# Kernel optimization log

Measured on AMD Instinct MI355X. Metric: run time of the kernel, lower is better.

## Reference

```python
import jax, jax.numpy as jnp
import numpy as np
import math

# Product of P Lorentz hyperboloids, each of dim D (time coord first), curvature c (K = 1/c).
N, P, D = 30000, 4, 64   # nodes, sub-manifolds, dim per sub-manifold
E = 480000               # edges (COO sparse adjacency)
C_IN, C_OUT = 1.0, 1.0
MIN_NORM = 1e-15
EPS = 1e-7
MAX_NORM = 1000.0


def _arcosh(x):
    return jnp.log(x + jnp.sqrt(jnp.maximum(x * x - 1.0, MIN_NORM)))


def proj(x, K):
    # project onto hyperboloid: recompute time coordinate from space coords
    y = x[..., 1:]
    t = jnp.sqrt(jnp.maximum(K + jnp.sum(y * y, -1, keepdims=True), EPS))
    return jnp.concatenate([t, y], -1)


def proj_tan0(u):
    # tangent space at origin: zero out the time coordinate
    return jnp.concatenate([jnp.zeros_like(u[..., :1]), u[..., 1:]], -1)


def proj_tan(u, x, K):
    ux = jnp.sum(x[..., 1:] * u[..., 1:], -1, keepdims=True)
    t = ux / jnp.maximum(x[..., :1], MIN_NORM)
    return jnp.concatenate([t, u[..., 1:]], -1)


def expmap0(u, K):
    sqrtK = K ** 0.5
    sp = u[..., 1:]
    n = jnp.maximum(jnp.linalg.norm(sp, axis=-1, keepdims=True), MIN_NORM)
    theta = n / sqrtK
    time = sqrtK * jnp.cosh(theta)
    space = sqrtK * jnp.sinh(theta) * sp / n
    return proj(jnp.concatenate([time, space], -1), K)


def logmap0(x, K):
    sqrtK = K ** 0.5
    sp = x[..., 1:]
    n = jnp.maximum(jnp.linalg.norm(sp, axis=-1, keepdims=True), MIN_NORM)
    theta = jnp.maximum(x[..., :1] / sqrtK, 1.0 + EPS)
    space = sqrtK * _arcosh(theta) * sp / n
    return jnp.concatenate([jnp.zeros_like(theta), space], -1)


def mink_dot(x, y):
    return jnp.sum(x[..., 1:] * y[..., 1:], -1, keepdims=True) - x[..., :1] * y[..., :1]


def expmap(u, x, K):
    sqrtK = K ** 0.5
    normu = jnp.minimum(jnp.sqrt(jnp.maximum(mink_dot(u, u), EPS)), MAX_NORM)
    theta = jnp.maximum(normu / sqrtK, MIN_NORM)
    return proj(jnp.cosh(theta) * x + jnp.sinh(theta) * u / theta, K)


def ptransp0(x, u, K):
    # parallel transport of tangent u at origin to point x
    sqrtK = K ** 0.5
    x0 = x[..., :1]
    y = x[..., 1:]
    yn = jnp.maximum(jnp.linalg.norm(y, axis=-1, keepdims=True), MIN_NORM)
    yu = y / yn
    v = jnp.concatenate([-yn, (sqrtK - x0) * yu], -1)
    alpha = jnp.sum(yu * u[..., 1:], -1, keepdims=True) / sqrtK
    return proj_tan(u - alpha * v, x, K)


def mobius_add(x, y, K):
    return expmap(ptransp0(x, logmap0(y, K), K), x, K)


def setup_inputs() -> dict:
    key = jax.random.key(0)
    k1, k2, k3, k4, k5 = jax.random.split(key, 5)
    K = 1.0 / C_IN
    # valid points on the product manifold: expmap0 of random tangent vectors
    t = 0.1 * jax.random.normal(k1, (N, P, D), dtype=jnp.float32)
    x = proj(expmap0(proj_tan0(t), K), K).reshape(N, P * D)
    adj_row = jax.random.randint(k2, (E,), 0, N)
    adj_col = jax.random.randint(k3, (E,), 0, N)
    # roughly degree-normalized positive adjacency weights
    adj_val = jax.random.uniform(k4, (E,), dtype=jnp.float32) / 16.0
    fan = P * D
    gain = math.sqrt(2.0) * math.sqrt(2.0 / (fan + fan))  # xavier_uniform(gain=sqrt(2)) scale
    weight = gain * jax.random.normal(k5, (fan, fan), dtype=jnp.float32)
    bias = jnp.full((fan,), 1e-4, dtype=jnp.float32)  # init.constant_(bias, 0.0001)
    return {"x": x, "adj_val": adj_val, "weight": weight, "bias": bias,
            "adj_row": adj_row, "adj_col": adj_col}


def reference(x, adj_val, weight, bias, adj_row, adj_col):
    K = 1.0 / C_IN
    Ko = 1.0 / C_OUT
    xs = x.reshape(N, P, D)

    # ---- ProLinear: mobius_matvec + hyperbolic bias add ----
    u = logmap0(xs, K).reshape(N, P * D)          # tangent at origin, concat across sub-manifolds
    mu = (u @ weight.T).reshape(N, P, D)          # [N, P*D] @ [P*D, P*D]^T
    h = proj(expmap0(proj_tan0(mu), K), K)
    b = bias.reshape(1, P, D)
    hyp_bias = proj(expmap0(proj_tan0(b), K), K)
    h = proj(mobius_add(h, hyp_bias, K), K)

    # ---- ProAgg: logmap0 -> spmm -> clamp -> expmap0 ----
    xt = logmap0(h, K).reshape(N, P * D)
    msgs = adj_val[:, None] * xt[adj_col]          # [E, P*D] gather
    support = jax.ops.segment_sum(msgs, adj_row, num_segments=N)
    support = jnp.minimum(support, MAX_NORM).reshape(N, P, D)
    h = proj(expmap0(proj_tan0(support), K), K)

    # ---- ProAct: logmap0 (c_in) -> clamped relu -> expmap0 (c_out) ----
    t = logmap0(h, K)
    t = jnp.minimum(jax.nn.relu(t), MAX_NORM)
    out = expmap0(proj_tan0(t), Ko)
    return out.reshape(N, P * D)
```

## Files before the change

kernel.cpp:

```cpp
#include <hip/hip_runtime.h>
#include <hip/hip_bf16.h>

#define MIN_NORM 1e-15f
#define EPS 1e-7f
#define MAX_NORM 1000.0f

#define NN 30000
#define PP 4
#define DD 64
#define EE 480000

typedef __attribute__((ext_vector_type(8))) short short8v;
typedef __attribute__((ext_vector_type(4))) float float4v;

__device__ inline float frcp(float x) { return __builtin_amdgcn_rcpf(x); }
__device__ inline float bf2f(unsigned short u) { return __uint_as_float(((unsigned)u) << 16); }
__device__ inline unsigned short f2bf(float f) {
    unsigned u = __float_as_uint(f);
    return (unsigned short)((u + 0x7fffu + ((u >> 16) & 1u)) >> 16);
}

__device__ inline float wsum(float v) {
#pragma unroll
    for (int off = 32; off >= 1; off >>= 1) v += __shfl_xor(v, off, 64);
    return v;
}
__device__ inline float expmap0_proj_pt(float v, int lane) {
    float sp = (lane == 0) ? 0.f : v;
    float n2 = wsum(sp * sp);
    float n = fmaxf(sqrtf(n2), MIN_NORM);
    float ep = __expf(n), em = frcp(ep);
    float s = 0.5f * (ep - em) * frcp(n);
    float time = sqrtf(fmaxf(1.f + s * s * n2, EPS));
    return (lane == 0) ? time : s * sp;
}
__device__ inline float logmap0_pt(float x, int lane) {
    float sp = (lane == 0) ? 0.f : x;
    float n2 = wsum(sp * sp);
    float n = fmaxf(sqrtf(n2), MIN_NORM);
    float x0 = __shfl(x, 0, 64);
    float th = fmaxf(x0, 1.f + EPS);
    float ac = __logf(th + sqrtf(fmaxf(th * th - 1.f, MIN_NORM)));
    return (lane == 0) ? 0.f : (ac * sp * frcp(n));
}
__device__ inline float gsum16(float v) {
#pragma unroll
    for (int off = 8; off >= 1; off >>= 1) v += __shfl_xor(v, off, 64);
    return v;
}
__device__ inline void gsum16x4(float& a, float& b, float& c, float& d) {
#pragma unroll
    for (int off = 8; off >= 1; off >>= 1) {
        a += __shfl_xor(a, off, 64);
        b += __shfl_xor(b, off, 64);
        c += __shfl_xor(c, off, 64);
        d += __shfl_xor(d, off, 64);
    }
}

__global__ void prep_kernel(const float* __restrict__ w,
                            unsigned short* __restrict__ bhi,
                            unsigned short* __restrict__ blo,
                            int* __restrict__ cz) {
    int b = blockIdx.x;
    if (b < 32) {
        int tt = b * 256 + threadIdx.x;
        int lane = tt & 63;
        int ks = (tt >> 6) & 7;
        int nt = tt >> 9;
        int col = nt * 16 + (lane & 15);
        int kb = ks * 32 + (lane >> 4) * 8;
#pragma unroll
        for (int e = 0; e < 8; e++) {
            float v = w[col * 256 + kb + e];
            unsigned short h = f2bf(v);
            bhi[tt * 8 + e] = h;
            blo[tt * 8 + e] = f2bf(v - bf2f(h));
        }
    } else {
        int i = (b - 32) * 256 + threadIdx.x;
        if (i < 2 * NN) cz[i] = 0;
    }
}

#define GR 16
#define UPITCH 264
__global__ __launch_bounds__(256) void fused_front_hist_kernel(const float* __restrict__ x,
                                                               const unsigned short* __restrict__ bhi,
                                                               const unsigned short* __restrict__ blo,
                                                               const float* __restrict__ bias,
                                                               unsigned short* __restrict__ xt,
                                                               const int* __restrict__ adj_row,
                                                               int* __restrict__ counts,
                                                               int nFront) {
    __shared__ __align__(16) char smem[17952];

    if (blockIdx.x >= nFront) {
        int e = (blockIdx.x - nFront) * 256 + threadIdx.x;
        if (e < EE) atomicAdd(&counts[adj_row[e]], 1);
        return;
    }

    unsigned short* uh = (unsigned short*)smem;
    unsigned short* ul = (unsigned short*)(smem + 8448);
    float* uspL = (float*)(smem + 16896);
    float* u2L  = (float*)(smem + 17920);

    int tid = threadIdx.x;
    int lane = tid & 63;
    int wv = tid >> 6;
    int row0 = blockIdx.x * GR;

    {
        float b = bias[wv * 64 + lane];
        float y = expmap0_proj_pt(b, lane);
        float usp = logmap0_pt(y, lane);
        float U2 = wsum(usp * usp);
        uspL[wv * 64 + lane] = usp;
        if (lane == 0) u2L[wv] = U2;
    }

    int r = tid >> 4, l = tid & 15;
    {
        const float4* xr = (const float4*)(x + (size_t)(row0 + r) * 256);
        float4 a[4];
#pragma unroll
        for (int p = 0; p < 4; p++) a[p] = xr[p * 16 + l];
        float s0, s1, s2, s3;
        {
            float m0 = (l == 0) ? 0.f : a[0].x;
            float m1 = (l == 0) ? 0.f : a[1].x;
            float m2 = (l == 0) ? 0.f : a[2].x;
            float m3 = (l == 0) ? 0.f : a[3].x;
            s0 = m0 * m0 + a[0].y * a[0].y + a[0].z * a[0].z + a[0].w * a[0].w;
            s1 = m1 * m1 + a[1].y * a[1].y + a[1].z * a[1].z + a[1].w * a[1].w;
            s2 = m2 * m2 + a[2].y * a[2].y + a[2].z * a[2].z + a[2].w * a[2].w;
            s3 = m3 * m3 + a[3].y * a[3].y + a[3].z * a[3].z + a[3].w * a[3].w;
        }
        gsum16x4(s0, s1, s2, s3);
        float n2a[4] = {s0, s1, s2, s3};
#pragma unroll
        for (int p = 0; p < 4; p++) {
            float n2 = n2a[p];
            float n = fmaxf(sqrtf(n2), MIN_NORM);
            float th = fmaxf(sqrtf(1.f + n2), 1.f + EPS);
            float ac = __logf(th + sqrtf(fmaxf(th * th - 1.f, MIN_NORM)));
            float sc = ac * frcp(n);
            float ux0 = (l == 0) ? 0.f : sc * a[p].x;
            float uy = sc * a[p].y, uz = sc * a[p].z, uw = sc * a[p].w;
            unsigned short hx = f2bf(ux0), hy = f2bf(uy), hz = f2bf(uz), hw = f2bf(uw);
            ushort4 hv = {hx, hy, hz, hw};
            ushort4 lv = {f2bf(ux0 - bf2f(hx)), f2bf(uy - bf2f(hy)),
                          f2bf(uz - bf2f(hz)), f2bf(uw - bf2f(hw))};
            *(ushort4*)(uh + r * UPITCH + p * 64 + 4 * l) = hv;
            *(ushort4*)(ul + r * UPITCH + p * 64 + 4 * l) = lv;
        }
    }
    __syncthreads();

    float4v acc[4];
#pragma unroll
    for (int j = 0; j < 4; j++) acc[j] = (float4v){0.f, 0.f, 0.f, 0.f};
    int abyte = (lane & 15) * (UPITCH * 2) + (lane >> 4) * 16;
#pragma unroll
    for (int ks = 0; ks < 8; ks++) {
        short8v Ah = *(const short8v*)(smem + abyte + ks * 64);
        short8v Al = *(const short8v*)(smem + 8448 + abyte + ks * 64);
#pragma unroll
        for (int j = 0; j < 4; j++) {
            size_t chunk = ((size_t)((wv * 4 + j) * 8 + ks) * 64 + lane) * 8;
            short8v Bh = *(const short8v*)(bhi + chunk);
            short8v Bl = *(const short8v*)(blo + chunk);
            acc[j] = __builtin_amdgcn_mfma_f32_16x16x32_bf16(Ah, Bh, acc[j], 0, 0, 0);
            acc[j] = __builtin_amdgcn_mfma_f32_16x16x32_bf16(Al, Bh, acc[j], 0, 0, 0);
            acc[j] = __builtin_amdgcn_mfma_f32_16x16x32_bf16(Ah, Bl, acc[j], 0, 0, 0);
        }
    }

    int lp = lane & 15, hi = lane >> 4;
    float uf[4];
#pragma unroll
    for (int j = 0; j < 4; j++) uf[j] = uspL[wv * 64 + j * 16 + lp];
    if (lp == 0) {
        acc[0][0] = 0.f; acc[0][1] = 0.f; acc[0][2] = 0.f; acc[0][3] = 0.f;
    }
    float n2v[4], duv[4];
#pragma unroll
    for (int reg = 0; reg < 4; reg++) {
        float pn = 0.f, pd = 0.f;
#pragma unroll
        for (int j = 0; j < 4; j++) {
            pn = fmaf(acc[j][reg], acc[j][reg], pn);
            pd = fmaf(acc[j][reg], uf[j], pd);
        }
        n2v[reg] = pn; duv[reg] = pd;
    }
#pragma unroll
    for (int off = 1; off < 16; off <<= 1) {
#pragma unroll
        for (int reg = 0; reg < 4; reg++) {
            n2v[reg] += __shfl_xor(n2v[reg], off, 64);
            duv[reg] += __shfl_xor(duv[reg], off, 64);
        }
    }
    float U2 = u2L[wv];

    float A[4], Bc[4];
#pragma unroll
    for (int reg = 0; reg < 4; reg++) {
        float n2 = n2v[reg], duu = duv[reg];
        float n = fmaxf(sqrtf(n2), MIN_NORM);
        float epv = __expf(n), emv = frcp(epv);
        float sv = 0.5f * (epv - emv) * frcp(n);
        float hs2 = sv * sv * n2;
        float h0 = sqrtf(fmaxf(1.f + hs2, EPS));
        float yn = fmaxf(sv * n, MIN_NORM);
        float dhu = sv * duu;
        float alpha = dhu * frcp(yn);
        float g = alpha * (1.f - h0);
        float ux = dhu - g * yn;
        float t = ux * frcp(fmaxf(h0, MIN_NORM));
        float w2 = U2 - 2.f * g * alpha + g * g;
        float md = w2 - t * t;
        float normu = fminf(sqrtf(fmaxf(md, EPS)), MAX_NORM);
        float theta = fmaxf(normu, MIN_NORM);
        float ep2 = __expf(theta), em2 = frcp(ep2);
        float ch = 0.5f * (ep2 + em2);
        float shot = 0.5f * (ep2 - em2) * frcp(theta);
        float rn2 = ch * ch * hs2 + 2.f * ch * shot * ux + shot * shot * w2;
        float rtime = sqrtf(fmaxf(1.f + rn2, EPS));
        float th2 = fmaxf(rtime, 1.f + EPS);
        float ac2 = __logf(th2 + sqrtf(fmaxf(th2 * th2 - 1.f, MIN_NORM)));
        float rn = fmaxf(sqrtf(rn2), MIN_NORM);
        float K = ac2 * frcp(rn);
        A[reg] = K * sv * (ch - shot * g * frcp(yn));
        Bc[reg] = K * shot;
    }

    unsigned short* xbase = xt + (size_t)(row0 + hi * 4) * 256 + wv * 64 + lp;
#pragma unroll
    for (int reg = 0; reg < 4; reg++) {
#pragma unroll
        for (int j = 0; j < 4; j++) {
            float o = fmaf(A[reg], acc[j][reg], Bc[reg] * uf[j]);
            xbase[reg * 256 + j * 16] = f2bf(o);
        }
    }
}

#define SCH 32
__global__ __launch_bounds__(1024) void scan_kernel(const int* __restrict__ counts,
                                                    int* __restrict__ starts, int n) {
    int tid = threadIdx.x, lane = tid & 63, wv = tid >> 6;
    int i0 = tid * SCH;
    int c[SCH];
    const int4* c4 = (const int4*)(counts + i0);
#pragma unroll
    for (int q = 0; q < 8; q++) {
        int4 v = c4[q];
        c[4 * q] = v.x; c[4 * q + 1] = v.y; c[4 * q + 2] = v.z; c[4 * q + 3] = v.w;
    }
    int s = 0;
#pragma unroll
    for (int j = 0; j < SCH; j++) s += c[j];
    int incl = s;
#pragma unroll
    for (int off = 1; off < 64; off <<= 1) {
        int t = __shfl_up(incl, off, 64);
        if (lane >= off) incl += t;
    }
    __shared__ int wtot[16];
    if (lane == 63) wtot[wv] = incl;
    __syncthreads();
    if (wv == 0 && lane < 16) {
        int v = wtot[lane];
        int sc = v;
#pragma unroll
        for (int off = 1; off < 16; off <<= 1) {
            int t = __shfl_up(sc, off, 64);
            if (lane >= off) sc += t;
        }
        wtot[lane] = sc - v;
    }
    __syncthreads();
    int run = incl - s + wtot[wv];
#pragma unroll
    for (int j = 0; j < SCH; j++) {
        int idx = i0 + j;
        if (idx < n) starts[idx] = run;
        run += c[j];
    }
    if (tid == 1023) starts[n] = run;
}

__global__ void scatter_kernel(const int* __restrict__ row, const int* __restrict__ col,
                               const float* __restrict__ val, const int* __restrict__ starts,
                               int* __restrict__ cursor, int2* __restrict__ ep, int E) {
    int e = blockIdx.x * 256 + threadIdx.x;
    if (e < E) {
        int r = row[e];
        int pos = starts[r] + atomicAdd(&cursor[r], 1);
        ep[pos] = make_int2(col[e], __float_as_int(val[e]));
    }
}

__global__ __launch_bounds__(256) void spmm_final_kernel(const unsigned short* __restrict__ xt,
                                                         const int2* __restrict__ ep,
                                                         const int* __restrict__ starts,
                                                         float4* __restrict__ out4) {
    int w = threadIdx.x >> 6;
    int lane = threadIdx.x & 63;
    int r = blockIdx.x * 4 + w;
    int s = starts[r], e = starts[r + 1];

    float4 acc = {0.f, 0.f, 0.f, 0.f};
    for (int i = s; i < e; i += 8) {
        int cs[8]; float vs[8];
#pragma unroll
        for (int u = 0; u < 8; u++) {
            int idx = i + u;
            bool ok = idx < e;
            int2 pe = ep[ok ? idx : s];
            cs[u] = pe.x;
            vs[u] = ok ? __int_as_float(pe.y) : 0.f;
        }
        ushort4 av[8];
#pragma unroll
        for (int u = 0; u < 8; u++)
            av[u] = *(const ushort4*)(xt + ((size_t)cs[u] << 8) + (lane << 2));
#pragma unroll
        for (int u = 0; u < 8; u++) {
            acc.x = fmaf(vs[u], bf2f(av[u].x), acc.x);
            acc.y = fmaf(vs[u], bf2f(av[u].y), acc.y);
            acc.z = fmaf(vs[u], bf2f(av[u].z), acc.z);
            acc.w = fmaf(vs[u], bf2f(av[u].w), acc.w);
        }
    }

    acc.x = fminf(acc.x, MAX_NORM); acc.y = fminf(acc.y, MAX_NORM);
    acc.z = fminf(acc.z, MAX_NORM); acc.w = fminf(acc.w, MAX_NORM);

    bool leader = ((lane & 15) == 0);
    float4 sp = acc;
    if (leader) sp.x = 0.f;
    float n2 = gsum16(sp.x * sp.x + sp.y * sp.y + sp.z * sp.z + sp.w * sp.w);
    float n = fmaxf(sqrtf(n2), MIN_NORM);
    float ep1 = __expf(n), em1 = frcp(ep1);
    float s1 = 0.5f * (ep1 - em1) * frcp(n);
    float hs2 = s1 * s1 * n2;
    float time = sqrtf(fmaxf(1.f + hs2, EPS));
    float th = fmaxf(time, 1.f + EPS);
    float ac = __logf(th + sqrtf(fmaxf(th * th - 1.f, MIN_NORM)));
    float hn = fmaxf(s1 * n, MIN_NORM);
    float sc = ac * s1 * frcp(hn);
    float4 t;
    t.x = leader ? 0.f : sc * sp.x;
    t.y = sc * sp.y;
    t.z = sc * sp.z;
    t.w = sc * sp.w;
    t.x = fminf(fmaxf(t.x, 0.f), MAX_NORM);
    t.y = fminf(fmaxf(t.y, 0.f), MAX_NORM);
    t.z = fminf(fmaxf(t.z, 0.f), MAX_NORM);
    t.w = fminf(fmaxf(t.w, 0.f), MAX_NORM);
    float t2 = gsum16(t.x * t.x + t.y * t.y + t.z * t.z + t.w * t.w);
    float nt = fmaxf(sqrtf(t2), MIN_NORM);
    float ep3 = __expf(nt), em3 = frcp(ep3);
    float s3 = 0.5f * (ep3 - em3) * frcp(nt);
    float time3 = sqrtf(fmaxf(1.f + s3 * s3 * t2, EPS));
    float4 o;
    o.x = leader ? time3 : s3 * t.x;
    o.y = s3 * t.y;
    o.z = s3 * t.z;
    o.w = s3 * t.w;

    out4[(size_t)r * 64 + lane] = o;
}

extern "C" void kernel_launch(void* const* d_in, const int* in_sizes, int n_in,
                              void* d_out, int out_size, void* d_ws, size_t ws_size,
                              hipStream_t stream) {
    const float* x       = (const float*)d_in[0];
    const float* adj_val = (const float*)d_in[1];
    const float* weight  = (const float*)d_in[2];
    const float* bias    = (const float*)d_in[3];
    const int*   adj_row = (const int*)d_in[4];
    const int*   adj_col = (const int*)d_in[5];

    const int N = NN, E = EE;

    unsigned short* B   = (unsigned short*)d_ws;
    unsigned short* Whi = B + (size_t)N * 256;
    unsigned short* Wlo = Whi + 65536;
    int* counts  = (int*)(Wlo + 65536);
    int* cursor  = counts + N;
    int* starts  = cursor + N;
    int2* ep     = (int2*)(starts + N + 2);

    const int nFront = N / GR;
    const int nHist  = (E + 255) / 256;

    prep_kernel<<<32 + (2 * N + 255) / 256, 256, 0, stream>>>(weight, Whi, Wlo, counts);
    fused_front_hist_kernel<<<nFront + nHist, 256, 0, stream>>>(x, Whi, Wlo, bias, B,
                                                                adj_row, counts, nFront);
    scan_kernel<<<1, 1024, 0, stream>>>(counts, starts, N);
    scatter_kernel<<<(E + 255) / 256, 256, 0, stream>>>(adj_row, adj_col, adj_val,
                                                        starts, cursor, ep, E);
    spmm_final_kernel<<<N / 4, 256, 0, stream>>>(B, ep, starts, (float4*)d_out);
}
```

Before: 146.5 us.

## Process 48 rows per front block and fold histogram into the same blocks

Each front block now handles 48 rows (three 16-row MFMA tiles) instead of 16, so every loaded B fragment of the split-bf16 weight is reused across three A tiles. The separate histogram blocks are removed; each front block instead atomically counts 768 edges (625 blocks x 768 = E exactly). The aim is to cut redundant weight fragment loads and launch fewer blocks, at the cost of about 51 KB of LDS per block, more accumulator registers, and reduced occupancy, with only 625 blocks in flight.

```diff
diff --git a/kernel.cpp b/kernel.cpp
--- a/kernel.cpp
+++ b/kernel.cpp
@@ -83,33 +83,33 @@
     }
 }
 
-#define GR 16
+#define GR 48
 #define UPITCH 264
+#define EPB 768
 __global__ __launch_bounds__(256) void fused_front_hist_kernel(const float* __restrict__ x,
                                                                const unsigned short* __restrict__ bhi,
                                                                const unsigned short* __restrict__ blo,
                                                                const float* __restrict__ bias,
                                                                unsigned short* __restrict__ xt,
                                                                const int* __restrict__ adj_row,
-                                                               int* __restrict__ counts,
-                                                               int nFront) {
-    __shared__ __align__(16) char smem[17952];
-
-    if (blockIdx.x >= nFront) {
-        int e = (blockIdx.x - nFront) * 256 + threadIdx.x;
-        if (e < EE) atomicAdd(&counts[adj_row[e]], 1);
-        return;
-    }
-
+                                                               int* __restrict__ counts) {
+    __shared__ __align__(16) char smem[51744];
     unsigned short* uh = (unsigned short*)smem;
-    unsigned short* ul = (unsigned short*)(smem + 8448);
-    float* uspL = (float*)(smem + 16896);
-    float* u2L  = (float*)(smem + 17920);
+    unsigned short* ul = (unsigned short*)(smem + 25344);
+    float* uspL = (float*)(smem + 50688);
+    float* u2L  = (float*)(smem + 51712);
 
     int tid = threadIdx.x;
     int lane = tid & 63;
     int wv = tid >> 6;
-    int row0 = blockIdx.x * GR;
+    int fb = blockIdx.x;
+    int row0 = fb * GR;
+
+    {
+        int e0 = fb * EPB + tid;
+#pragma unroll
+        for (int q = 0; q < 3; q++) atomicAdd(&counts[adj_row[e0 + q * 256]], 1);
+    }
 
     {
         float b = bias[wv * 64 + lane];
@@ -122,58 +122,74 @@
 
     int r = tid >> 4, l = tid & 15;
     {
-        const float4* xr = (const float4*)(x + (size_t)(row0 + r) * 256);
-        float4 a[4];
-#pragma unroll
-        for (int p = 0; p < 4; p++) a[p] = xr[p * 16 + l];
-        float s0, s1, s2, s3;
-        {
-            float m0 = (l == 0) ? 0.f : a[0].x;
-            float m1 = (l == 0) ? 0.f : a[1].x;
-            float m2 = (l == 0) ? 0.f : a[2].x;
-            float m3 = (l == 0) ? 0.f : a[3].x;
-            s0 = m0 * m0 + a[0].y * a[0].y + a[0].z * a[0].z + a[0].w * a[0].w;
-            s1 = m1 * m1 + a[1].y * a[1].y + a[1].z * a[1].z + a[1].w * a[1].w;
-            s2 = m2 * m2 + a[2].y * a[2].y + a[2].z * a[2].z + a[2].w * a[2].w;
-            s3 = m3 * m3 + a[3].y * a[3].y + a[3].z * a[3].z + a[3].w * a[3].w;
-        }
-        gsum16x4(s0, s1, s2, s3);
-        float n2a[4] = {s0, s1, s2, s3};
-#pragma unroll
-        for (int p = 0; p < 4; p++) {
-            float n2 = n2a[p];
-            float n = fmaxf(sqrtf(n2), MIN_NORM);
-            float th = fmaxf(sqrtf(1.f + n2), 1.f + EPS);
-            float ac = __logf(th + sqrtf(fmaxf(th * th - 1.f, MIN_NORM)));
-            float sc = ac * frcp(n);
-            float ux0 = (l == 0) ? 0.f : sc * a[p].x;
-            float uy = sc * a[p].y, uz = sc * a[p].z, uw = sc * a[p].w;
-            unsigned short hx = f2bf(ux0), hy = f2bf(uy), hz = f2bf(uz), hw = f2bf(uw);
-            ushort4 hv = {hx, hy, hz, hw};
-            ushort4 lv = {f2bf(ux0 - bf2f(hx)), f2bf(uy - bf2f(hy)),
-                          f2bf(uz - bf2f(hz)), f2bf(uw - bf2f(hw))};
-            *(ushort4*)(uh + r * UPITCH + p * 64 + 4 * l) = hv;
-            *(ushort4*)(ul + r * UPITCH + p * 64 + 4 * l) = lv;
+        float4 a[3][4];
+#pragma unroll
+        for (int rr = 0; rr < 3; rr++) {
+            const float4* xr = (const float4*)(x + (size_t)(row0 + rr * 16 + r) * 256);
+#pragma unroll
+            for (int p = 0; p < 4; p++) a[rr][p] = xr[p * 16 + l];
+        }
+#pragma unroll
+        for (int rr = 0; rr < 3; rr++) {
+            float s0, s1, s2, s3;
+            {
+                float m0 = (l == 0) ? 0.f : a[rr][0].x;
+                float m1 = (l == 0) ? 0.f : a[rr][1].x;
+                float m2 = (l == 0) ? 0.f : a[rr][2].x;
+                float m3 = (l == 0) ? 0.f : a[rr][3].x;
+                s0 = m0 * m0 + a[rr][0].y * a[rr][0].y + a[rr][0].z * a[rr][0].z + a[rr][0].w * a[rr][0].w;
+                s1 = m1 * m1 + a[rr][1].y * a[rr][1].y + a[rr][1].z * a[rr][1].z + a[rr][1].w * a[rr][1].w;
+                s2 = m2 * m2 + a[rr][2].y * a[rr][2].y + a[rr][2].z * a[rr][2].z + a[rr][2].w * a[rr][2].w;
+                s3 = m3 * m3 + a[rr][3].y * a[rr][3].y + a[rr][3].z * a[rr][3].z + a[rr][3].w * a[rr][3].w;
+            }
+            gsum16x4(s0, s1, s2, s3);
+            float n2a[4] = {s0, s1, s2, s3};
+            int rowbase = (rr * 16 + r) * UPITCH;
+#pragma unroll
+            for (int p = 0; p < 4; p++) {
+                float n2 = n2a[p];
+                float n = fmaxf(sqrtf(n2), MIN_NORM);
+                float th = fmaxf(sqrtf(1.f + n2), 1.f + EPS);
+                float ac = __logf(th + sqrtf(fmaxf(th * th - 1.f, MIN_NORM)));
+                float sc = ac * frcp(n);
+                float ux0 = (l == 0) ? 0.f : sc * a[rr][p].x;
+                float uy = sc * a[rr][p].y, uz = sc * a[rr][p].z, uw = sc * a[rr][p].w;
+                unsigned short hx = f2bf(ux0), hy = f2bf(uy), hz = f2bf(uz), hw = f2bf(uw);
+                ushort4 hv = {hx, hy, hz, hw};
+                ushort4 lv = {f2bf(ux0 - bf2f(hx)), f2bf(uy - bf2f(hy)),
+                              f2bf(uz - bf2f(hz)), f2bf(uw - bf2f(hw))};
+                *(ushort4*)(uh + rowbase + p * 64 + 4 * l) = hv;
+                *(ushort4*)(ul + rowbase + p * 64 + 4 * l) = lv;
+            }
         }
     }
     __syncthreads();
 
-    float4v acc[4];
-#pragma unroll
-    for (int j = 0; j < 4; j++) acc[j] = (float4v){0.f, 0.f, 0.f, 0.f};
+    float4v acc[3][4];
+#pragma unroll
+    for (int m = 0; m < 3; m++)
+#pragma unroll
+        for (int j = 0; j < 4; j++) acc[m][j] = (float4v){0.f, 0.f, 0.f, 0.f};
     int abyte = (lane & 15) * (UPITCH * 2) + (lane >> 4) * 16;
 #pragma unroll
     for (int ks = 0; ks < 8; ks++) {
-        short8v Ah = *(const short8v*)(smem + abyte + ks * 64);
-        short8v Al = *(const short8v*)(smem + 8448 + abyte + ks * 64);
+        short8v Ah[3], Al[3];
+#pragma unroll
+        for (int m = 0; m < 3; m++) {
+            Ah[m] = *(const short8v*)(smem + abyte + m * 8448 + ks * 64);
+            Al[m] = *(const short8v*)(smem + 25344 + abyte + m * 8448 + ks * 64);
+        }
 #pragma unroll
         for (int j = 0; j < 4; j++) {
             size_t chunk = ((size_t)((wv * 4 + j) * 8 + ks) * 64 + lane) * 8;
             short8v Bh = *(const short8v*)(bhi + chunk);
             short8v Bl = *(const short8v*)(blo + chunk);
-            acc[j] = __builtin_amdgcn_mfma_f32_16x16x32_bf16(Ah, Bh, acc[j], 0, 0, 0);
-            acc[j] = __builtin_amdgcn_mfma_f32_16x16x32_bf16(Al, Bh, acc[j], 0, 0, 0);
-            acc[j] = __builtin_amdgcn_mfma_f32_16x16x32_bf16(Ah, Bl, acc[j], 0, 0, 0);
+#pragma unroll
+            for (int m = 0; m < 3; m++) {
+                acc[m][j] = __builtin_amdgcn_mfma_f32_16x16x32_bf16(Ah[m], Bh, acc[m][j], 0, 0, 0);
+                acc[m][j] = __builtin_amdgcn_mfma_f32_16x16x32_bf16(Al[m], Bh, acc[m][j], 0, 0, 0);
+                acc[m][j] = __builtin_amdgcn_mfma_f32_16x16x32_bf16(Ah[m], Bl, acc[m][j], 0, 0, 0);
+            }
         }
     }
 
@@ -181,69 +197,71 @@
     float uf[4];
 #pragma unroll
     for (int j = 0; j < 4; j++) uf[j] = uspL[wv * 64 + j * 16 + lp];
-    if (lp == 0) {
-        acc[0][0] = 0.f; acc[0][1] = 0.f; acc[0][2] = 0.f; acc[0][3] = 0.f;
-    }
-    float n2v[4], duv[4];
-#pragma unroll
-    for (int reg = 0; reg < 4; reg++) {
-        float pn = 0.f, pd = 0.f;
-#pragma unroll
-        for (int j = 0; j < 4; j++) {
-            pn = fmaf(acc[j][reg], acc[j][reg], pn);
-            pd = fmaf(acc[j][reg], uf[j], pd);
-        }
-        n2v[reg] = pn; duv[reg] = pd;
-    }
-#pragma unroll
-    for (int off = 1; off < 16; off <<= 1) {
+    float U2 = u2L[wv];
+
+#pragma unroll
+    for (int m = 0; m < 3; m++) {
+        if (lp == 0) {
+            acc[m][0][0] = 0.f; acc[m][0][1] = 0.f; acc[m][0][2] = 0.f; acc[m][0][3] = 0.f;
+        }
+        float n2v[4], duv[4];
 #pragma unroll
         for (int reg = 0; reg < 4; reg++) {
-            n2v[reg] += __shfl_xor(n2v[reg], off, 64);
-            duv[reg] += __shfl_xor(duv[reg], off, 64);
-        }
-    }
-    float U2 = u2L[wv];
-
-    float A[4], Bc[4];
-#pragma unroll
-    for (int reg = 0; reg < 4; reg++) {
-        float n2 = n2v[reg], duu = duv[reg];
-        float n = fmaxf(sqrtf(n2), MIN_NORM);
-        float epv = __expf(n), emv = frcp(epv);
-        float sv = 0.5f * (epv - emv) * frcp(n);
-        float hs2 = sv * sv * n2;
-        float h0 = sqrtf(fmaxf(1.f + hs2, EPS));
-        float yn = fmaxf(sv * n, MIN_NORM);
-        float dhu = sv * duu;
-        float alpha = dhu * frcp(yn);
-        float g = alpha * (1.f - h0);
-        float ux = dhu - g * yn;
-        float t = ux * frcp(fmaxf(h0, MIN_NORM));
-        float w2 = U2 - 2.f * g * alpha + g * g;
-        float md = w2 - t * t;
-        float normu = fminf(sqrtf(fmaxf(md, EPS)), MAX_NORM);
-        float theta = fmaxf(normu, MIN_NORM);
-        float ep2 = __expf(theta), em2 = frcp(ep2);
-        float ch = 0.5f * (ep2 + em2);
-        float shot = 0.5f * (ep2 - em2) * frcp(theta);
-        float rn2 = ch * ch * hs2 + 2.f * ch * shot * ux + shot * shot * w2;
-        float rtime = sqrtf(fmaxf(1.f + rn2, EPS));
-        float th2 = fmaxf(rtime, 1.f + EPS);
-        float ac2 = __logf(th2 + sqrtf(fmaxf(th2 * th2 - 1.f, MIN_NORM)));
-        float rn = fmaxf(sqrtf(rn2), MIN_NORM);
-        float K = ac2 * frcp(rn);
-        A[reg] = K * sv * (ch - shot * g * frcp(yn));
-        Bc[reg] = K * shot;
-    }
-
-    unsigned short* xbase = xt + (size_t)(row0 + hi * 4) * 256 + wv * 64 + lp;
-#pragma unroll
-    for (int reg = 0; reg < 4; reg++) {
-#pragma unroll
-        for (int j = 0; j < 4; j++) {
-            float o = fmaf(A[reg], acc[j][reg], Bc[reg] * uf[j]);
-            xbase[reg * 256 + j * 16] = f2bf(o);
+            float pn = 0.f, pd = 0.f;
+#pragma unroll
+            for (int j = 0; j < 4; j++) {
+                pn = fmaf(acc[m][j][reg], acc[m][j][reg], pn);
+                pd = fmaf(acc[m][j][reg], uf[j], pd);
+            }
+            n2v[reg] = pn; duv[reg] = pd;
+        }
+#pragma unroll
+        for (int off = 1; off < 16; off <<= 1) {
+#pragma unroll
+            for (int reg = 0; reg < 4; reg++) {
+                n2v[reg] += __shfl_xor(n2v[reg], off, 64);
+                duv[reg] += __shfl_xor(duv[reg], off, 64);
+            }
+        }
+        float A[4], Bc[4];
+#pragma unroll
+        for (int reg = 0; reg < 4; reg++) {
+            float n2 = n2v[reg], duu = duv[reg];
+            float n = fmaxf(sqrtf(n2), MIN_NORM);
+            float epv = __expf(n), emv = frcp(epv);
+            float sv = 0.5f * (epv - emv) * frcp(n);
+            float hs2 = sv * sv * n2;
+            float h0 = sqrtf(fmaxf(1.f + hs2, EPS));
+            float yn = fmaxf(sv * n, MIN_NORM);
+            float dhu = sv * duu;
+            float alpha = dhu * frcp(yn);
+            float g = alpha * (1.f - h0);
+            float ux = dhu - g * yn;
+            float t = ux * frcp(fmaxf(h0, MIN_NORM));
+            float w2 = U2 - 2.f * g * alpha + g * g;
+            float md = w2 - t * t;
+            float normu = fminf(sqrtf(fmaxf(md, EPS)), MAX_NORM);
+            float theta = fmaxf(normu, MIN_NORM);
+            float ep2 = __expf(theta), em2 = frcp(ep2);
+            float ch = 0.5f * (ep2 + em2);
+            float shot = 0.5f * (ep2 - em2) * frcp(theta);
+            float rn2 = ch * ch * hs2 + 2.f * ch * shot * ux + shot * shot * w2;
+            float rtime = sqrtf(fmaxf(1.f + rn2, EPS));
+            float th2 = fmaxf(rtime, 1.f + EPS);
+            float ac2 = __logf(th2 + sqrtf(fmaxf(th2 * th2 - 1.f, MIN_NORM)));
+            float rn = fmaxf(sqrtf(rn2), MIN_NORM);
+            float K = ac2 * frcp(rn);
+            A[reg] = K * sv * (ch - shot * g * frcp(yn));
+            Bc[reg] = K * shot;
+        }
+        unsigned short* xbase = xt + (size_t)(row0 + m * 16 + hi * 4) * 256 + wv * 64 + lp;
+#pragma unroll
+        for (int reg = 0; reg < 4; reg++) {
+#pragma unroll
+            for (int j = 0; j < 4; j++) {
+                float o = fmaf(A[reg], acc[m][j][reg], Bc[reg] * uf[j]);
+                xbase[reg * 256 + j * 16] = f2bf(o);
+            }
         }
     }
 }
@@ -396,12 +414,9 @@
     int* starts  = cursor + N;
     int2* ep     = (int2*)(starts + N + 2);
 
-    const int nFront = N / GR;
-    const int nHist  = (E + 255) / 256;
-
     prep_kernel<<<32 + (2 * N + 255) / 256, 256, 0, stream>>>(weight, Whi, Wlo, counts);
-    fused_front_hist_kernel<<<nFront + nHist, 256, 0, stream>>>(x, Whi, Wlo, bias, B,
-                                                                adj_row, counts, nFront);
+    fused_front_hist_kernel<<<N / GR, 256, 0, stream>>>(x, Whi, Wlo, bias, B,
+                                                        adj_row, counts);
     scan_kernel<<<1, 1024, 0, stream>>>(counts, starts, N);
     scatter_kernel<<<(E + 255) / 256, 256, 0, stream>>>(adj_row, adj_col, adj_val,
                                                         starts, cursor, ep, E);
```

New measurement: 146.4 us. About the same (-0.1%).
